# Kernel tuning notes

Hardware: AMD Instinct MI355X
Metric: run time of the kernel (lower is better)

Reference implementation:

```python
import jax, jax.numpy as jnp
import numpy as np
from jax import lax

RADIUS = 2
TOP_K = 4096
TEMP = 0.1
K_SIZE = 2 * RADIUS + 1   # 5
K2 = K_SIZE * K_SIZE      # 25


def _maxpool(x, r):
    # torch max_pool2d pads implicitly with -inf
    k = 2 * r + 1
    return lax.reduce_window(x, -jnp.inf, lax.max,
                             (1, 1, k, k), (1, 1, 1, 1),
                             [(0, 0), (0, 0), (r, r), (r, r)])


def simple_nms(scores, r):
    zeros = jnp.zeros_like(scores)
    max_mask = scores == _maxpool(scores, r)
    for _ in range(2):
        supp_mask = _maxpool(max_mask.astype(scores.dtype), r) > 0
        supp_scores = jnp.where(supp_mask, zeros, scores)
        new_max_mask = supp_scores == _maxpool(supp_scores, r)
        max_mask = max_mask | (new_max_mask & ~supp_mask)
    return jnp.where(max_mask, scores, zeros)


def setup_inputs() -> dict:
    key = jax.random.key(0)
    scores_map = jax.random.uniform(key, (8, 1, 1024, 1024), dtype=jnp.float32)
    return {"scores_map": scores_map}


def reference(scores_map):
    b, c, h, w = scores_map.shape
    r = RADIUS
    dtype = scores_map.dtype

    scores_nograd = lax.stop_gradient(scores_map)
    nms = simple_nms(scores_nograd, r)
    # zero out borders (image_size is None branch)
    nms = nms.at[:, :, :r, :].set(0).at[:, :, :, :r].set(0)
    nms = nms.at[:, :, -r:, :].set(0).at[:, :, :, -r:].set(0)

    # top_k > 0 branch: fixed-size keypoint selection per image
    _, idx = lax.top_k(nms.reshape(b, -1), TOP_K)   # [b, K]
    ky = idx // w
    kx = idx % w

    # hw_grid: meshgrid(ij) of linspace(-r, r), flattened row-major, cols swapped -> (dx, dy)
    lin = jnp.linspace(-r, r, K_SIZE).astype(dtype)
    gi, gj = jnp.meshgrid(lin, lin, indexing='ij')          # gi = dy offsets, gj = dx offsets
    hw_grid = jnp.stack([gj.ravel(), gi.ravel()], axis=1)   # [K2, 2] (x, y)

    # gather 5x5 patches around each keypoint (== unfold with zero padding)
    dy = jnp.repeat(jnp.arange(K_SIZE), K_SIZE)   # [K2] row-major: dy outer
    dx = jnp.tile(jnp.arange(K_SIZE), K_SIZE)     # dx inner, matches unfold/hw_grid order
    padded = jnp.pad(scores_map[:, 0], ((0, 0), (r, r), (r, r)))  # [b, h+2r, w+2r]

    def gather_b(p, yy, xx):
        return p[yy[:, None] + dy[None, :], xx[:, None] + dx[None, :]]  # [K, K2]

    patches = jax.vmap(gather_b)(padded, ky, kx)  # [b, K, K2]

    # soft-argmax with detached max for numerical stability
    max_v = lax.stop_gradient(patches.max(axis=-1, keepdims=True))
    x_exp = jnp.exp((patches - max_v) / TEMP)
    ssum = x_exp.sum(axis=-1)                                 # [b, K]
    xy_residual = jnp.einsum('bkp,pd->bkd', x_exp, hw_grid) / ssum[..., None]  # [b, K, 2]

    dist2 = (((hw_grid[None, None, :, :] - xy_residual[:, :, None, :]) / r) ** 2).sum(-1)  # [b,K,K2]
    scoredispersity = (x_exp * dist2).sum(axis=-1) / ssum     # [b, K]

    xy_nms = jnp.stack([kx, ky], axis=-1).astype(dtype)       # [b, K, 2]
    wh = jnp.array([w - 1, h - 1], dtype=dtype)
    keypoints = (xy_nms + xy_residual) / wh * 2 - 1           # normalized to [-1, 1]

    # bilinear grid_sample, align_corners=True
    px = (keypoints[..., 0] + 1) * 0.5 * (w - 1)
    py = (keypoints[..., 1] + 1) * 0.5 * (h - 1)
    fx = jnp.floor(px)
    fy = jnp.floor(py)
    wx = px - fx
    wy = py - fy
    x0 = jnp.clip(fx, 0, w - 1).astype(jnp.int32)
    x1 = jnp.clip(fx + 1, 0, w - 1).astype(jnp.int32)
    y0 = jnp.clip(fy, 0, h - 1).astype(jnp.int32)
    y1 = jnp.clip(fy + 1, 0, h - 1).astype(jnp.int32)

    def sample_b(img, a0, a1, b0, b1):
        return img[a0, b0], img[a0, b1], img[a1, b0], img[a1, b1]

    v00, v01, v10, v11 = jax.vmap(sample_b)(scores_map[:, 0], y0, y1, x0, x1)
    kptscores = (v00 * (1 - wx) * (1 - wy) + v01 * wx * (1 - wy)
                 + v10 * (1 - wx) * wy + v11 * wx * wy)       # [b, K]

    return keypoints, scoredispersity, kptscores
```

## Files before the change

### kernel.cpp

```cpp
#include <hip/hip_runtime.h>
#include <math.h>

#define H 1024
#define W 1024
#define B 8
#define TOPK 4096
#define CAP 131072
#define NBT 8192
#define NCH 16
#define GK 20480
#define TILE_X 108
#define TILE_Y 108
#define GDX 10
#define GDY 10
#define SKCAP 2048

typedef unsigned long long u64;
typedef unsigned int u32;
typedef unsigned short u16;

__device__ __forceinline__ float dpp_up1(float v) {
    int r = __builtin_amdgcn_update_dpp(0, __float_as_int(v), 0x138, 0xF, 0xF, true);
    return __int_as_float(r);
}
__device__ __forceinline__ float dpp_dn1(float v) {
    int r = __builtin_amdgcn_update_dpp(0, __float_as_int(v), 0x130, 0xF, 0xF, true);
    return __int_as_float(r);
}

__device__ __forceinline__ int binOf(u64 key) {
    u32 fb = (u32)(key >> 32);
    u32 ex = fb >> 23;
    if (ex >= 0x7Fu) return NBT - 1;
    if (ex == 0x7Eu) {
        u32 m13 = (fb >> 10) & 0x1FFFu;
        return (m13 < 64u) ? 64 : (int)m13;
    }
    if (ex >= 0x6Eu) return (int)(ex - 0x6Eu + 47u);
    return 1;
}

#define ROUND_A(VR0, VR1, USE_SUPP)                                               \
    _Pragma("unroll") for (int i = 0; i < 16; ++i) {                              \
        int r = rbase + i;                                                        \
        if (r < (VR0) || r > (VR1)) continue;                                     \
        float x = svx[i], y = svy[i];                                             \
        if (USE_SUPP) {                                                           \
            u64 se = sp[r][0], so = sp[r][1];                                     \
            u32 s0 = (u32)(se >> lane) & 1u;                                      \
            u32 s1 = (u32)(so >> lane) & 1u;                                      \
            sbx |= s0 << i;                                                       \
            sby |= s1 << i;                                                       \
            if (s0) x = 0.0f;                                                     \
            if (s1) y = 0.0f;                                                     \
        }                                                                         \
        float ux = dpp_up1(x), uy = dpp_up1(y);                                   \
        float dxx = dpp_dn1(x), dyy = dpp_dn1(y);                                 \
        float m01 = fmaxf(x, y);                                                  \
        float h0 = fmaxf(fmaxf(ux, uy), fmaxf(m01, dxx));                         \
        float h1 = fmaxf(fmaxf(uy, m01), fmaxf(dxx, dyy));                        \
        h0r[i] = h0;                                                              \
        h1r[i] = h1;                                                              \
        if (i == 0 || i == 1 || i == 14 || i == 15) {                             \
            int k = (i < 2) ? i : i - 12;                                         \
            *(float2*)&hb[w * 4 + k][2 * lane] = make_float2(h0, h1);             \
        }                                                                         \
    }

#define GATHER_V()                                                                \
        float v0x, v0y, v1x, v1y, v3x, v3y, v4x, v4y;                             \
        if (i >= 2) { v0x = h0r[i - 2]; v0y = h1r[i - 2]; }                       \
        else { int k = (i == 0) ? 2 : 3;                                          \
               float2 t = *(const float2*)&hb[(w - 1) * 4 + k][2 * lane];         \
               v0x = t.x; v0y = t.y; }                                            \
        if (i >= 1) { v1x = h0r[i - 1]; v1y = h1r[i - 1]; }                       \
        else { float2 t = *(const float2*)&hb[(w - 1) * 4 + 3][2 * lane];         \
               v1x = t.x; v1y = t.y; }                                            \
        if (i <= 14) { v3x = h0r[i + 1]; v3y = h1r[i + 1]; }                      \
        else { float2 t = *(const float2*)&hb[(w + 1) * 4 + 0][2 * lane];         \
               v3x = t.x; v3y = t.y; }                                            \
        if (i <= 13) { v4x = h0r[i + 2]; v4y = h1r[i + 2]; }                      \
        else { int k = (i == 14) ? 0 : 1;                                         \
               float2 t = *(const float2*)&hb[(w + 1) * 4 + k][2 * lane];         \
               v4x = t.x; v4y = t.y; }

#define ROUND_B(VV0, VV1, USE_SUPP, FIRST)                                        \
    _Pragma("unroll") for (int i = 0; i < 16; ++i) {                              \
        int r = rbase + i;                                                        \
        if (r < (VV0) || r > (VV1)) continue;                                     \
        GATHER_V()                                                                \
        float vm0 = fmaxf(fmaxf(fmaxf(v0x, v1x), fmaxf(v3x, v4x)), h0r[i]);       \
        float vm1 = fmaxf(fmaxf(fmaxf(v0y, v1y), fmaxf(v3y, v4y)), h1r[i]);       \
        float x = svx[i], y = svy[i];                                             \
        bool sb0 = false, sb1 = false;                                            \
        if (USE_SUPP) {                                                           \
            sb0 = (sbx >> i) & 1u;                                                \
            sb1 = (sby >> i) & 1u;                                                \
            if (sb0) x = 0.0f;                                                    \
            if (sb1) y = 0.0f;                                                    \
        }                                                                         \
        int c0 = 2 * lane;                                                        \
        bool bit0 = (x == vm0) && !sb0 && (svx[i] != -INFINITY) &&                \
                    c0 >= (VV0) && c0 <= (VV1);                                   \
        bool bit1 = (y == vm1) && !sb1 && (svy[i] != -INFINITY) &&                \
                    (c0 + 1) >= (VV0) && (c0 + 1) <= (VV1);                       \
        u64 bE = __ballot(bit0), bO = __ballot(bit1);                             \
        if (lane == 0) {                                                          \
            u64 ne = ((FIRST) ? 0ull : ma[r][0]) | bE;                            \
            u64 no = ((FIRST) ? 0ull : ma[r][1]) | bO;                            \
            ma[r][0] = ne;                                                        \
            ma[r][1] = no;                                                        \
        }                                                                         \
    }

#define ROUND_B_FINAL()                                                           \
    _Pragma("unroll") for (int i = 0; i < 16; ++i) {                              \
        int r = rbase + i;                                                        \
        if (r < 10 || r > 117) continue;                                          \
        GATHER_V()                                                                \
        float vm0 = fmaxf(fmaxf(fmaxf(v0x, v1x), fmaxf(v3x, v4x)), h0r[i]);       \
        float vm1 = fmaxf(fmaxf(fmaxf(v0y, v1y), fmaxf(v3y, v4y)), h1r[i]);       \
        float x = svx[i], y = svy[i];                                             \
        bool sb0 = (sbx >> i) & 1u;                                               \
        bool sb1 = (sby >> i) & 1u;                                               \
        if (sb0) x = 0.0f;                                                        \
        if (sb1) y = 0.0f;                                                        \
        int c0 = 2 * lane;                                                        \
        bool bit0 = (x == vm0) && !sb0 && (svx[i] != -INFINITY);                  \
        bool bit1 = (y == vm1) && !sb1 && (svy[i] != -INFINITY);                  \
        u64 me_old = ma[r][0], mo_old = ma[r][1];                                 \
        bool fin0 = bit0 || (((me_old >> lane) & 1ull) != 0);                     \
        bool fin1 = bit1 || (((mo_old >> lane) & 1ull) != 0);                     \
        int gy = gy0 + r;                                                         \
        if (c0 >= 10 && c0 <= 117 && fin0 && svx[i] > 0.0f &&                     \
            gx >= 2 && gx < W - 2 && gy >= 2 && gy < H - 2) {                     \
            u32 pos = atomicAdd(&lcnt, 1u);                                       \
            if (pos < SKCAP) {                                                    \
                u32 p = (u32)(gy * W + gx);                                       \
                skey[pos] = ((u64)__float_as_uint(svx[i]) << 32) | (u64)(~p);     \
            }                                                                     \
        }                                                                         \
        if (c0 + 1 >= 10 && c0 + 1 <= 117 && fin1 && svy[i] > 0.0f &&             \
            gx + 1 >= 2 && gx + 1 < W - 2 && gy >= 2 && gy < H - 2) {             \
            u32 pos = atomicAdd(&lcnt, 1u);                                       \
            if (pos < SKCAP) {                                                    \
                u32 p = (u32)(gy * W + gx + 1);                                   \
                skey[pos] = ((u64)__float_as_uint(svy[i]) << 32) | (u64)(~p);     \
            }                                                                     \
        }                                                                         \
    }

#define DILATE(R0, R1)                                                            \
    if (tid >= (R0) && tid <= (R1)) {                                             \
        int rr = tid;                                                             \
        u64 e = ma[rr - 2][0] | ma[rr - 1][0] | ma[rr][0] | ma[rr + 1][0] |       \
                ma[rr + 2][0];                                                    \
        u64 o = ma[rr - 2][1] | ma[rr - 1][1] | ma[rr][1] | ma[rr + 1][1] |       \
                ma[rr + 2][1];                                                    \
        sp[rr][0] = e | (e << 1) | (e >> 1) | o | (o << 1);                       \
        sp[rr][1] = o | (o << 1) | (o >> 1) | e | (e >> 1);                       \
    }

__global__ __launch_bounds__(512) void k_nms(const float* __restrict__ scores,
                                             u64* __restrict__ surv,
                                             u32* __restrict__ cnt) {
    __shared__ float hb[32][128];
    __shared__ __align__(16) u64 ma[128][2];
    __shared__ __align__(16) u64 sp[128][2];
    __shared__ u64 skey[SKCAP];
    __shared__ u32 lcnt, gbase;
    const int b = blockIdx.z;
    const int gx0 = blockIdx.x * TILE_X - 10;
    const int gy0 = blockIdx.y * TILE_Y - 10;
    const float* img = scores + (size_t)b * H * W;
    const int tid = (int)threadIdx.x, lane = tid & 63, w = tid >> 6, rbase = w * 16;
    const int gx = gx0 + 2 * lane;
    if (tid == 0) lcnt = 0;

    float svx[16], svy[16], h0r[16], h1r[16];
    u32 sbx = 0, sby = 0;
#pragma unroll
    for (int i = 0; i < 16; ++i) {
        int gy = gy0 + rbase + i;
        float x = -INFINITY, y = -INFINITY;
        if (gy >= 0 && gy < H) {
            const float* row = img + (size_t)gy * W;
            if (gx >= 0 && gx + 1 < W) {
                float2 t = *(const float2*)(row + gx);
                x = t.x; y = t.y;
            } else if (gx >= 0 && gx < W) {
                x = row[gx];
            }
        }
        svx[i] = x; svy[i] = y;
    }

    ROUND_A(0, 127, false)
    __syncthreads();
    ROUND_B(2, 125, false, 1)
    __syncthreads();
    DILATE(4, 123)
    __syncthreads();
    sbx = 0; sby = 0;
    ROUND_A(4, 123, true)
    __syncthreads();
    ROUND_B(6, 121, true, 0)
    __syncthreads();
    DILATE(8, 119)
    __syncthreads();
    sbx = 0; sby = 0;
    ROUND_A(8, 119, true)
    __syncthreads();
    ROUND_B_FINAL()
    __syncthreads();
    u32 nk = lcnt < SKCAP ? lcnt : SKCAP;
    if (tid == 0) gbase = nk ? atomicAdd(&cnt[b], nk) : 0u;
    __syncthreads();
    for (u32 i = tid; i < nk; i += 512)
        surv[(size_t)b * CAP + gbase + i] = skey[i];
}

__global__ __launch_bounds__(512) void k_hist(const u64* __restrict__ surv,
                                              const u32* __restrict__ cnt,
                                              u16* __restrict__ M) {
    __shared__ u32 h[NBT];
    int img = blockIdx.x / NCH, c = blockIdx.x % NCH;
    int tid = (int)threadIdx.x;
    for (int i = tid; i < NBT; i += 512) h[i] = 0;
    __syncthreads();
    u32 n = cnt[img];
    if (n > CAP) n = CAP;
    u32 chunk = (n + NCH - 1) / NCH;
    u32 lo = c * chunk, hi = min(n, lo + chunk);
    const u64* sv = surv + (size_t)img * CAP;
    for (u32 i = lo + tid; i < hi; i += 512) atomicAdd(&h[binOf(sv[i])], 1u);
    __syncthreads();
    u16* dst = M + ((size_t)img * NCH + c) * NBT;
    for (int i = tid; i < NBT; i += 512) dst[i] = (u16)h[i];
}

__global__ __launch_bounds__(1024) void k_scan(const u16* __restrict__ M,
                                               u32* __restrict__ offC,
                                               u32* __restrict__ basetot,
                                               int* __restrict__ tinfo,
                                               u64* __restrict__ gkeys) {
    __shared__ u32 wsum[16];
    __shared__ u32 sh_ntot;
    __shared__ int sh_T;
    __shared__ u32 sh_r, sh_m;
    int img = blockIdx.x, tid = (int)threadIdx.x;
    const u16* Mi = M + (size_t)img * NCH * NBT;
    const int base = NBT - 8 - tid * 8;
    u32 reg[8] = {0, 0, 0, 0, 0, 0, 0, 0};
    for (int c = 0; c < NCH; ++c) {
        const u16* p = Mi + (size_t)c * NBT + base;
        ushort4 a = *(const ushort4*)(p);
        ushort4 b2 = *(const ushort4*)(p + 4);
        reg[0] += a.x; reg[1] += a.y; reg[2] += a.z; reg[3] += a.w;
        reg[4] += b2.x; reg[5] += b2.y; reg[6] += b2.z; reg[7] += b2.w;
    }
    u32 tot = 0;
#pragma unroll
    for (int j = 0; j < 8; ++j) tot += reg[j];
    u32 x = tot;
    int ln = tid & 63, wv = tid >> 6;
#pragma unroll
    for (int off = 1; off < 64; off <<= 1) {
        u32 v = (u32)__shfl_up((int)x, off);
        if (ln >= off) x += v;
    }
    if (ln == 63) wsum[wv] = x;
    __syncthreads();
    if (tid < 16) {
        u32 wval = wsum[tid];
        u32 wx = wval;
        for (int off = 1; off < 16; off <<= 1) {
            u32 v = (u32)__shfl_up((int)wx, off);
            if (tid >= off) wx += v;
        }
        wsum[tid] = wx - wval;
        if (tid == 15) sh_ntot = wx;
    }
    __syncthreads();
    u32 incl = x + wsum[wv];
    u32 excl = incl - tot;
    u32 ntot = sh_ntot;
    if (ntot > TOPK) {
        if (excl < TOPK && TOPK <= incl) {
            u32 cum = excl;
#pragma unroll
            for (int j = 0; j < 8; ++j) {
                u32 cj = reg[7 - j];
                if (cum + cj >= TOPK) {
                    sh_T = NBT - 1 - tid * 8 - j;
                    sh_r = TOPK - cum;
                    sh_m = cj;
                    break;
                }
                cum += cj;
            }
        }
    } else if (tid == 0) { sh_T = -1; sh_r = 0; sh_m = 0; }
    __syncthreads();
    int T = sh_T;
    int TT = (T < 0) ? 0 : T;
    u32* offi = offC + (size_t)img * NBT * NCH;
    u32* bti = basetot + (size_t)img * NBT;
    u32 cum = excl;
    int hi = NBT - 1 - tid * 8;
#pragma unroll
    for (int j = 0; j < 8; ++j) {
        int bin = hi - j;
        u32 c0 = reg[7 - j];
        if (bin > T) {
            u32 run = cum;
            for (int c = 0; c < NCH; ++c) {
                offi[(size_t)(bin - TT) * NCH + c] = run;
                run += Mi[(size_t)c * NBT + bin];
            }
            bti[bin] = (cum << 16) | c0;
        } else if (bin == T && T >= 0) {
            u32 run = TOPK;
            for (int c = 0; c < NCH; ++c) {
                offi[(size_t)(bin - TT) * NCH + c] = run;
                run += Mi[(size_t)c * NBT + bin];
            }
        }
        cum += c0;
    }
    u64* gk = gkeys + (size_t)img * GK;
    for (int i = tid; i < TOPK; i += 1024) gk[i] = 0ull;
    if (tid == 0) {
        tinfo[3 * img] = T;
        tinfo[3 * img + 1] = (int)sh_r;
        tinfo[3 * img + 2] = (int)sh_m;
    }
}

__global__ __launch_bounds__(512) void k_scatter(const u64* __restrict__ surv,
                                                 const u32* __restrict__ cnt,
                                                 const int* __restrict__ tinfo,
                                                 const u32* __restrict__ offC,
                                                 u64* __restrict__ gkeys) {
    __shared__ u32 loff[NBT];
    int img = blockIdx.x / NCH, c = blockIdx.x % NCH;
    int tid = (int)threadIdx.x;
    int T = tinfo[3 * img];
    int TT = (T < 0) ? 0 : T;
    int R = NBT - TT;
    const u32* src = offC + (size_t)img * NBT * NCH;
    for (int i = tid; i < R; i += 512) loff[i] = src[(size_t)i * NCH + c];
    __syncthreads();
    u32 n = cnt[img];
    if (n > CAP) n = CAP;
    u32 chunk = (n + NCH - 1) / NCH;
    u32 lo = c * chunk, hiX = min(n, lo + chunk);
    const u64* sv = surv + (size_t)img * CAP;
    u64* gk = gkeys + (size_t)img * GK;
    for (u32 i = lo + tid; i < hiX; i += 512) {
        u64 kk = sv[i];
        int bb = binOf(kk);
        if (bb < TT) continue;
        u32 slot = atomicAdd(&loff[bb - TT], 1u);
        if (slot < GK) gk[slot] = kk;
    }
}

__global__ __launch_bounds__(1024) void k_fin(const int* __restrict__ tinfo,
                                              const u32* __restrict__ basetot,
                                              const u64* __restrict__ gkeys,
                                              u64* __restrict__ sorted) {
    __shared__ u64 up[TOPK];
    __shared__ u64 cnd[4096];
    int img = blockIdx.x, tid = (int)threadIdx.x;
    int T = tinfo[3 * img];
    u32 r = (u32)tinfo[3 * img + 1];
    u32 m = (u32)tinfo[3 * img + 2];
    if (m > 4096u) m = 4096u;
    const u64* gk = gkeys + (size_t)img * GK;
    for (int i = tid; i < TOPK; i += 1024) up[i] = gk[i];
    for (u32 i = tid; i < m; i += 1024) cnd[i] = gk[TOPK + i];
    __syncthreads();
    u64* dst = sorted + (size_t)img * TOPK;
    for (u32 i = tid; i < m; i += 1024) {
        u64 ki = cnd[i];
        u32 g = 0;
        for (u32 j = 0; j < m; ++j) g += (cnd[j] > ki) ? 1u : 0u;
        if (g < r) dst[TOPK - r + g] = ki;
    }
    u32 upper = TOPK - r;
    const u32* bti = basetot + (size_t)img * NBT;
    for (u32 s = tid; s < upper; s += 1024) {
        u64 kk = up[s];
        if (kk == 0ull) { dst[s] = 0ull; continue; }
        int bb = binOf(kk);
        u32 v = bti[bb];
        u32 base = v >> 16, cc = v & 0xFFFFu;
        u32 g = 0;
        for (u32 j = 0; j < cc; ++j) g += (up[base + j] > kk) ? 1u : 0u;
        dst[base + g] = kk;
    }
}

__global__ __launch_bounds__(256) void k_out(const float* __restrict__ scores,
                                             const u64* __restrict__ sorted,
                                             float* __restrict__ out) {
    int gtid = blockIdx.x * 256 + (int)threadIdx.x;
    int wid = gtid >> 6;
    int l = gtid & 63;
    int half = l >> 5;
    int c = l & 31;
    int kpg = wid * 2 + half;
    int b = kpg >> 12;
    int kp = kpg & (TOPK - 1);
    const float* img = scores + (size_t)b * H * W;
    u64 key = sorted[(size_t)b * TOPK + kp];
    u32 idx = ~(u32)(key & 0xFFFFFFFFull);
    int ky = (int)(idx >> 10) & 1023, kx = (int)(idx & 1023);
    ky = min(max(ky, 2), H - 3);
    kx = min(max(kx, 2), W - 3);
    int row = c / 5, col = c % 5;
    float v = 0.0f;
    if (c < 25) v = img[(ky + row - 2) * W + (kx + col - 2)];
    float mx = (c < 25) ? v : -INFINITY;
#pragma unroll
    for (int mk = 1; mk < 32; mk <<= 1) mx = fmaxf(mx, __shfl_xor(mx, mk));
    float e = (c < 25) ? expf((v - mx) / 0.1f) : 0.0f;
    float dxv = (float)(col - 2), dyv = (float)(row - 2);
    float s0 = e, s1 = e * dxv, s2 = e * dyv;
#pragma unroll
    for (int mk = 1; mk < 32; mk <<= 1) {
        s0 += __shfl_xor(s0, mk);
        s1 += __shfl_xor(s1, mk);
        s2 += __shfl_xor(s2, mk);
    }
    float xr = s1 / s0, yr = s2 / s0;
    float ddx = (dxv - xr) * 0.5f, ddy = (dyv - yr) * 0.5f;
    float d = e * (ddx * ddx + ddy * ddy);
#pragma unroll
    for (int mk = 1; mk < 32; mk <<= 1) d += __shfl_xor(d, mk);
    float disp = d / s0;
    float kpx = ((float)kx + xr) / 1023.0f * 2.0f - 1.0f;
    float kpy = ((float)ky + yr) / 1023.0f * 2.0f - 1.0f;
    float px = (kpx + 1.0f) * 0.5f * 1023.0f;
    float py = (kpy + 1.0f) * 0.5f * 1023.0f;
    float fx = floorf(px), fy = floorf(py);
    float wx = px - fx, wy = py - fy;
    int x0 = (int)fminf(fmaxf(fx, 0.f), 1023.f);
    int x1 = (int)fminf(fmaxf(fx + 1.f, 0.f), 1023.f);
    int y0 = (int)fminf(fmaxf(fy, 0.f), 1023.f);
    int y1 = (int)fminf(fmaxf(fy + 1.f, 0.f), 1023.f);
    float bv = 0.0f;
    if (c < 4) {
        int xx = (c & 1) ? x1 : x0;
        int yy = (c >> 1) ? y1 : y0;
        bv = img[yy * W + xx];
    }
    int base = half * 32;
    float v00 = __shfl(bv, base + 0);
    float v01 = __shfl(bv, base + 1);
    float v10 = __shfl(bv, base + 2);
    float v11 = __shfl(bv, base + 3);
    float sc = v00 * (1.f - wx) * (1.f - wy) + v01 * wx * (1.f - wy) +
               v10 * (1.f - wx) * wy + v11 * wx * wy;
    if (c == 0) {
        size_t kb = (size_t)b * TOPK + kp;
        out[kb * 2 + 0] = kpx;
        out[kb * 2 + 1] = kpy;
        out[(size_t)B * TOPK * 2 + kb] = disp;
        out[(size_t)B * TOPK * 3 + kb] = sc;
    }
}

extern "C" void kernel_launch(void* const* d_in, const int* in_sizes, int n_in,
                              void* d_out, int out_size, void* d_ws, size_t ws_size,
                              hipStream_t stream) {
    const float* scores = (const float*)d_in[0];
    float* out = (float*)d_out;
    char* ws = (char*)d_ws;
    u64* surv = (u64*)ws;
    u16* M = (u16*)(ws + 8388608);
    u32* offC = (u32*)(ws + 10485760);
    u32* basetot = (u32*)(ws + 14680064);
    u64* gkeys = (u64*)(ws + 15204352);
    u64* sorted = (u64*)(ws + 16515072);
    u32* cnt = (u32*)(ws + 16777216);
    int* tinfo = (int*)(ws + 16777280);

    hipMemsetAsync(cnt, 0, B * sizeof(u32), stream);

    k_nms<<<dim3(GDX, GDY, B), 512, 0, stream>>>(scores, surv, cnt);
    k_hist<<<B * NCH, 512, 0, stream>>>(surv, cnt, M);
    k_scan<<<B, 1024, 0, stream>>>(M, offC, basetot, tinfo, gkeys);
    k_scatter<<<B * NCH, 512, 0, stream>>>(surv, cnt, tinfo, offC, gkeys);
    k_fin<<<B, 1024, 0, stream>>>(tinfo, basetot, gkeys, sorted);
    k_out<<<(B * TOPK * 32) / 256, 256, 0, stream>>>(scores, sorted, out);
}
```

Before: 105.8 us.

## Split final rank-sort across 17 blocks per image, reading keys from global

The final ranking kernel goes from one 1024-thread block per image to 17 blocks of 256 threads per image. Sixteen blocks rank the upper keys within their bins and one block ranks the threshold-bin candidates. Shared-memory staging is dropped and the comparison loops read keys directly from global memory, relying on cache. The aim is to fill more compute units in a kernel that previously ran only 8 blocks. The trade-off is more global or cache traffic in the O(m^2) candidate loop, which now runs on a single 256-thread block, and the candidate cap is raised from 4096 to GK-TOPK.

```diff
diff --git a/kernel.cpp b/kernel.cpp
--- a/kernel.cpp
+++ b/kernel.cpp
@@ -366,39 +366,43 @@
     }
 }
 
-__global__ __launch_bounds__(1024) void k_fin(const int* __restrict__ tinfo,
-                                              const u32* __restrict__ basetot,
-                                              const u64* __restrict__ gkeys,
-                                              u64* __restrict__ sorted) {
-    __shared__ u64 up[TOPK];
-    __shared__ u64 cnd[4096];
-    int img = blockIdx.x, tid = (int)threadIdx.x;
+__global__ __launch_bounds__(256) void k_fin(const int* __restrict__ tinfo,
+                                             const u32* __restrict__ basetot,
+                                             const u64* __restrict__ gkeys,
+                                             u64* __restrict__ sorted) {
+    int img = blockIdx.x / 17;
+    int slice = blockIdx.x % 17;
+    int tid = (int)threadIdx.x;
     int T = tinfo[3 * img];
     u32 r = (u32)tinfo[3 * img + 1];
     u32 m = (u32)tinfo[3 * img + 2];
-    if (m > 4096u) m = 4096u;
+    if (m > (u32)(GK - TOPK)) m = (u32)(GK - TOPK);
     const u64* gk = gkeys + (size_t)img * GK;
-    for (int i = tid; i < TOPK; i += 1024) up[i] = gk[i];
-    for (u32 i = tid; i < m; i += 1024) cnd[i] = gk[TOPK + i];
-    __syncthreads();
+    const u32* bti = basetot + (size_t)img * NBT;
     u64* dst = sorted + (size_t)img * TOPK;
-    for (u32 i = tid; i < m; i += 1024) {
-        u64 ki = cnd[i];
-        u32 g = 0;
-        for (u32 j = 0; j < m; ++j) g += (cnd[j] > ki) ? 1u : 0u;
-        if (g < r) dst[TOPK - r + g] = ki;
-    }
-    u32 upper = TOPK - r;
-    const u32* bti = basetot + (size_t)img * NBT;
-    for (u32 s = tid; s < upper; s += 1024) {
-        u64 kk = up[s];
-        if (kk == 0ull) { dst[s] = 0ull; continue; }
-        int bb = binOf(kk);
-        u32 v = bti[bb];
-        u32 base = v >> 16, cc = v & 0xFFFFu;
-        u32 g = 0;
-        for (u32 j = 0; j < cc; ++j) g += (up[base + j] > kk) ? 1u : 0u;
-        dst[base + g] = kk;
+    if (slice < 16) {
+        u32 s = (u32)(slice * 256 + tid);
+        u32 upper = TOPK - r;
+        if (s < upper) {
+            u64 kk = gk[s];
+            if (kk == 0ull) {
+                dst[s] = 0ull;
+            } else {
+                int bb = binOf(kk);
+                u32 v = bti[bb];
+                u32 base = v >> 16, cc = v & 0xFFFFu;
+                u32 g = 0;
+                for (u32 j = 0; j < cc; ++j) g += (gk[base + j] > kk) ? 1u : 0u;
+                dst[base + g] = kk;
+            }
+        }
+    } else {
+        for (u32 i = (u32)tid; i < m; i += 256) {
+            u64 ki = gk[TOPK + i];
+            u32 g = 0;
+            for (u32 j = 0; j < m; ++j) g += (gk[TOPK + j] > ki) ? 1u : 0u;
+            if (g < r) dst[TOPK - r + g] = ki;
+        }
     }
 }
 
@@ -493,6 +497,6 @@
     k_hist<<<B * NCH, 512, 0, stream>>>(surv, cnt, M);
     k_scan<<<B, 1024, 0, stream>>>(M, offC, basetot, tinfo, gkeys);
     k_scatter<<<B * NCH, 512, 0, stream>>>(surv, cnt, tinfo, offC, gkeys);
-    k_fin<<<B, 1024, 0, stream>>>(tinfo, basetot, gkeys, sorted);
+    k_fin<<<B * 17, 256, 0, stream>>>(tinfo, basetot, gkeys, sorted);
     k_out<<<(B * TOPK * 32) / 256, 256, 0, stream>>>(scores, sorted, out);
 }
```

New measurement: 102.8 us. 1.03x faster.
